# Performance work log

Measured on AMD Instinct MI355X. Metric: run time of the kernel, lower is better.

Reference implementation:

```python
import jax, jax.numpy as jnp
import numpy as np

T, N, E = 12, 100000, 3200000
F = H = 64
O, L = 32, 2


def setup_inputs() -> dict:
    key = jax.random.key(0)
    ks = jax.random.split(key, 13)
    sc = 0.08  # keep gate pre-activations in a sane range
    return {
        "x": jax.random.normal(ks[0], (T, N, F), jnp.float32),
        "hidden_states": jax.random.normal(ks[1], (L, N, H), jnp.float32),
        "cell_states": jax.random.normal(ks[2], (L, N, H), jnp.float32),
        "Wx_self": jax.random.normal(ks[3], (L, 4, F, H), jnp.float32) * sc,
        "Wx_neigh": jax.random.normal(ks[4], (L, 4, F, H), jnp.float32) * sc,
        "Wh_self": jax.random.normal(ks[5], (L, 4, H, H), jnp.float32) * sc,
        "Wh_neigh": jax.random.normal(ks[6], (L, 4, H, H), jnp.float32) * sc,
        "w_c": jax.random.normal(ks[7], (L, 3, H), jnp.float32) * sc,  # peephole i,f,o
        "bias": jax.random.normal(ks[8], (L, 4, H), jnp.float32) * sc,  # i,f,c,o
        "Wout": jax.random.normal(ks[9], (H, O), jnp.float32) * sc,
        "bout": jax.random.normal(ks[10], (O,), jnp.float32) * sc,
        "src": jax.random.randint(ks[11], (E,), 0, N, jnp.int32),
        "dst": jax.random.randint(ks[12], (E,), 0, N, jnp.int32),
    }


def reference(x, hidden_states, cell_states, Wx_self, Wx_neigh, Wh_self,
              Wh_neigh, w_c, bias, Wout, bout, src, dst):
    # mean aggregation over incoming edges (DGL copy_u + mean reduce)
    deg = jax.ops.segment_sum(jnp.ones((E,), x.dtype), dst, num_segments=N)
    deg_inv = jnp.where(deg > 0, 1.0 / deg, 0.0)[:, None]  # [N,1]

    def mean_agg(feat):  # [N,D] -> [N,D]
        return jax.ops.segment_sum(feat[src], dst, num_segments=N) * deg_inv

    def gates(feat, agg, Ws, Wn):  # Ws,Wn: [4,D,H] -> [4,N,H]
        return (jnp.einsum('nf,gfh->gnh', feat, Ws)
                + jnp.einsum('nf,gfh->gnh', agg, Wn))

    def step(carry, x_t):
        hs, cs = carry  # [L,N,H] each
        inp = x_t
        new_h, new_c = [], []
        for j in range(L):
            h, c = hs[j], cs[j]
            x_agg = mean_agg(inp)  # reuse_msg_passing: one agg shared by 4 gates
            h_agg = mean_agg(h)
            pre = gates(inp, x_agg, Wx_self[j], Wx_neigh[j]) \
                + gates(h, h_agg, Wh_self[j], Wh_neigh[j])  # [4,N,H]
            i = jax.nn.sigmoid(pre[0] + w_c[j, 0] * c + bias[j, 0])
            f = jax.nn.sigmoid(pre[1] + w_c[j, 1] * c + bias[j, 1])
            c_tilde = jnp.tanh(pre[2] + bias[j, 2])
            nc = f * c + i * c_tilde
            o = jax.nn.sigmoid(pre[3] + w_c[j, 2] * nc + bias[j, 3])
            nh = o * jnp.tanh(nc)
            new_h.append(nh)
            new_c.append(nc)
            inp = nh
        out_t = inp @ Wout + bout  # [N,O]
        return (jnp.stack(new_h), jnp.stack(new_c)), out_t

    (h_f, c_f), outs = jax.lax.scan(step, (hidden_states, cell_states), x)
    return outs, h_f, c_f  # outs: [T,N,O]
```

## Files before the change

kernel.cpp:

```cpp
#include <hip/hip_runtime.h>

#define T_STEPS 12
#define NN 100000
#define EE 3200000
#define HD 64
#define OD 32
#define NBK 391

typedef __attribute__((ext_vector_type(8))) short short8;
typedef __attribute__((ext_vector_type(4))) float f32x4;
typedef __attribute__((ext_vector_type(2))) float f32x2;
typedef unsigned short u16;
typedef unsigned char u8;

__device__ __forceinline__ u16 f2b(float x) {
  union { float f; unsigned u; } v; v.f = x;
  unsigned r = v.u + 0x7FFFu + ((v.u >> 16) & 1u);
  return (u16)(r >> 16);
}
__device__ __forceinline__ float b2f(u16 u) {
  union { unsigned u; float f; } v; v.u = ((unsigned)u) << 16;
  return v.f;
}
__device__ __forceinline__ float sigm(float x) {
  x = fminf(fmaxf(x, -30.f), 30.f);
  return 1.0f / (1.0f + __expf(-x));
}
__device__ __forceinline__ float tanh_f(float x) {
  x = fminf(fmaxf(x, -15.f), 15.f);
  float e = __expf(2.0f * x);
  return (e - 1.0f) / (e + 1.0f);
}

__device__ __forceinline__ uint2 pack8_fp8(const float* f) {
  unsigned lo = 0, hi = 0;
  lo = __builtin_amdgcn_cvt_pk_fp8_f32(f[0], f[1], lo, false);
  lo = __builtin_amdgcn_cvt_pk_fp8_f32(f[2], f[3], lo, true);
  hi = __builtin_amdgcn_cvt_pk_fp8_f32(f[4], f[5], hi, false);
  hi = __builtin_amdgcn_cvt_pk_fp8_f32(f[6], f[7], hi, true);
  return make_uint2(lo, hi);
}
__device__ __forceinline__ u8 f2q(float x) {
  return (u8)(__builtin_amdgcn_cvt_pk_fp8_f32(x, 0.f, 0u, false) & 0xFFu);
}
__device__ __forceinline__ void acc8_fp8(uint2 v, float* a) {
  f32x2 p0 = __builtin_amdgcn_cvt_pk_f32_fp8(v.x, false);
  f32x2 p1 = __builtin_amdgcn_cvt_pk_f32_fp8(v.x, true);
  f32x2 p2 = __builtin_amdgcn_cvt_pk_f32_fp8(v.y, false);
  f32x2 p3 = __builtin_amdgcn_cvt_pk_f32_fp8(v.y, true);
  a[0] += p0[0]; a[1] += p0[1]; a[2] += p1[0]; a[3] += p1[1];
  a[4] += p2[0]; a[5] += p2[1]; a[6] += p3[0]; a[7] += p3[1];
}

__global__ __launch_bounds__(256) void k_bhist(const int* __restrict__ dst,
                                               int* __restrict__ bcnt, int E) {
  __shared__ int h[NBK];
  for (int i = threadIdx.x; i < NBK; i += 256) h[i] = 0;
  __syncthreads();
  int base = blockIdx.x * 4096;
#pragma unroll
  for (int i = 0; i < 16; ++i) {
    int e = base + i * 256 + threadIdx.x;
    if (e < E) atomicAdd(&h[dst[e] >> 8], 1);
  }
  __syncthreads();
  for (int i = threadIdx.x; i < NBK; i += 256)
    if (h[i]) atomicAdd(&bcnt[i], h[i]);
}

__global__ __launch_bounds__(512) void k_bscan(const int* __restrict__ bcnt,
                                               int* __restrict__ bcur) {
  __shared__ int buf[512];
  int tid = threadIdx.x;
  int v = (tid < NBK) ? bcnt[tid] : 0;
  buf[tid] = v;
  __syncthreads();
  for (int off = 1; off < 512; off <<= 1) {
    int t = (tid >= off) ? buf[tid - off] : 0;
    __syncthreads();
    buf[tid] += t;
    __syncthreads();
  }
  if (tid < NBK) bcur[tid] = buf[tid] - v;
}

__global__ __launch_bounds__(256) void k_bscatter(const int* __restrict__ src,
                                                  const int* __restrict__ dst,
                                                  int* __restrict__ bcur,
                                                  uint2* __restrict__ binned, int E) {
  __shared__ int h[NBK];
  __shared__ int base[NBK];
  __shared__ int cur[NBK];
  for (int i = threadIdx.x; i < NBK; i += 256) { h[i] = 0; cur[i] = 0; }
  __syncthreads();
  int b0 = blockIdx.x * 4096;
  int d[16], s[16];
#pragma unroll
  for (int i = 0; i < 16; ++i) {
    int e = b0 + i * 256 + threadIdx.x;
    if (e < E) {
      d[i] = dst[e];
      s[i] = src[e];
      atomicAdd(&h[d[i] >> 8], 1);
    } else d[i] = -1;
  }
  __syncthreads();
  for (int i = threadIdx.x; i < NBK; i += 256)
    if (h[i]) base[i] = atomicAdd(&bcur[i], h[i]);
  __syncthreads();
#pragma unroll
  for (int i = 0; i < 16; ++i) {
    if (d[i] >= 0) {
      int bk = d[i] >> 8;
      int r = atomicAdd(&cur[bk], 1);
      binned[base[bk] + r] = make_uint2((unsigned)s[i], (unsigned)d[i]);
    }
  }
}

__global__ __launch_bounds__(256) void k_count2(const uint2* __restrict__ binned,
                                                int* __restrict__ deg, int E) {
  int e = blockIdx.x * 256 + threadIdx.x;
  if (e < E) atomicAdd(&deg[binned[e].y], 1);
}

__global__ __launch_bounds__(1024) void k_scanA(const int* __restrict__ deg,
                                                int* __restrict__ excl,
                                                int* __restrict__ btot, int n) {
  __shared__ int buf[1024];
  int tid = threadIdx.x;
  int i = blockIdx.x * 1024 + tid;
  int v = (i < n) ? deg[i] : 0;
  buf[tid] = v;
  __syncthreads();
  for (int off = 1; off < 1024; off <<= 1) {
    int t = (tid >= off) ? buf[tid - off] : 0;
    __syncthreads();
    buf[tid] += t;
    __syncthreads();
  }
  if (i < n) excl[i] = buf[tid] - v;
  if (tid == 1023) btot[blockIdx.x] = buf[1023];
}

__global__ __launch_bounds__(128) void k_scanB(const int* __restrict__ btot,
                                               int* __restrict__ boffs, int nb) {
  __shared__ int buf[128];
  int tid = threadIdx.x;
  int v = (tid < nb) ? btot[tid] : 0;
  buf[tid] = v;
  __syncthreads();
  for (int off = 1; off < 128; off <<= 1) {
    int t = (tid >= off) ? buf[tid - off] : 0;
    __syncthreads();
    buf[tid] += t;
    __syncthreads();
  }
  if (tid < nb) boffs[tid] = buf[tid] - v;
}

__global__ __launch_bounds__(1024) void k_scanC(const int* __restrict__ deg,
                                                const int* __restrict__ excl,
                                                const int* __restrict__ boffs,
                                                int* __restrict__ row_ptr,
                                                int* __restrict__ cursor,
                                                float* __restrict__ deg_inv, int n) {
  int i = blockIdx.x * 1024 + threadIdx.x;
  if (i < n) {
    int v = excl[i] + boffs[blockIdx.x];
    int d = deg[i];
    row_ptr[i] = v;
    cursor[i] = v;
    deg_inv[i] = d ? (1.0f / (float)d) : 0.0f;
    if (i == n - 1) row_ptr[n] = v + d;
  }
}

__global__ __launch_bounds__(256) void k_scatter2(const uint2* __restrict__ binned,
                                                  int* __restrict__ cursor,
                                                  int* __restrict__ csr, int E) {
  int e = blockIdx.x * 256 + threadIdx.x;
  if (e < E) {
    uint2 p = binned[e];
    int pos = atomicAdd(&cursor[p.y], 1);
    csr[pos] = (int)p.x;
  }
}

__global__ __launch_bounds__(256) void k_prep(const float* __restrict__ Wxs,
                                              const float* __restrict__ Wxn,
                                              const float* __restrict__ Whs,
                                              const float* __restrict__ Whn,
                                              u16* __restrict__ bprep) {
  int idx = blockIdx.x * 256 + threadIdx.x;
  int l = idx >> 16;
  int kb = (idx >> 13) & 7;
  int fi = (idx >> 9) & 15;
  int ln = (idx >> 3) & 63;
  int j = idx & 7;
  int fc = kb * 32 + ((ln >> 4) << 3) + j;
  int g = fi & 3;
  int kk = ((fi >> 2) << 4) + (ln & 15);
  int t = fc >> 6, f = fc & 63;
  const float* tabs[4] = {Wxs, Wxn, Whs, Whn};
  bprep[idx] = f2b(tabs[t][((size_t)(l * 4 + g) * 64 + f) * 64 + kk]);
}

__global__ __launch_bounds__(256) void k_prepw(const float* __restrict__ Wout,
                                               u16* __restrict__ wp) {
  int idx = blockIdx.x * 256 + threadIdx.x;
  int kb = idx >> 10;
  int fi = (idx >> 9) & 1;
  int ln = (idx >> 3) & 63;
  int j = idx & 7;
  int k = kb * 32 + ((ln >> 4) << 3) + j;
  int o = fi * 16 + (ln & 15);
  wp[idx] = f2b(Wout[k * 32 + o]);
}

__global__ __launch_bounds__(256) void k_convx(const float* __restrict__ x,
                                               u16* __restrict__ pa,
                                               u8* __restrict__ paq) {
  int idx = blockIdx.x * 256 + threadIdx.x;
  int n = idx >> 3, j = idx & 7;
  float4 v0 = *reinterpret_cast<const float4*>(x + (size_t)n * 64 + j * 8);
  float4 v1 = *reinterpret_cast<const float4*>(x + (size_t)n * 64 + j * 8 + 4);
  float f[8] = {v0.x, v0.y, v0.z, v0.w, v1.x, v1.y, v1.z, v1.w};
  short8 o;
#pragma unroll
  for (int i = 0; i < 8; ++i) o[i] = (short)f2b(f[i]);
  *reinterpret_cast<short8*>(pa + (size_t)n * 128 + j * 8) = o;
  *reinterpret_cast<uint2*>(paq + (size_t)n * 128 + j * 8) = pack8_fp8(f);
}

__global__ __launch_bounds__(256) void k_inith(const float* __restrict__ h0,
                                               u16* __restrict__ H0,
                                               u8* __restrict__ H0q,
                                               u16* __restrict__ PA,
                                               u8* __restrict__ PAq) {
  int idx = blockIdx.x * 256 + threadIdx.x;
  int n = idx >> 3, j = idx & 7;
#pragma unroll
  for (int L = 0; L < 2; ++L) {
    float4 v0 = *reinterpret_cast<const float4*>(h0 + (size_t)L * NN * 64 + (size_t)n * 64 + j * 8);
    float4 v1 = *reinterpret_cast<const float4*>(h0 + (size_t)L * NN * 64 + (size_t)n * 64 + j * 8 + 4);
    float f[8] = {v0.x, v0.y, v0.z, v0.w, v1.x, v1.y, v1.z, v1.w};
    short8 o;
#pragma unroll
    for (int i = 0; i < 8; ++i) o[i] = (short)f2b(f[i]);
    uint2 q = pack8_fp8(f);
    if (L == 0) {
      *reinterpret_cast<short8*>(H0 + (size_t)n * 64 + j * 8) = o;
      *reinterpret_cast<uint2*>(H0q + (size_t)n * 64 + j * 8) = q;
    } else {
      *reinterpret_cast<short8*>(PA + (size_t)n * 128 + 64 + j * 8) = o;
      *reinterpret_cast<uint2*>(PAq + (size_t)n * 128 + 64 + j * 8) = q;
    }
  }
}

__global__ __launch_bounds__(256) void k_agg_pair(const u8* __restrict__ Q,
                                                  const int* __restrict__ row_ptr,
                                                  const int* __restrict__ csr,
                                                  const float* __restrict__ deg_inv,
                                                  u16* __restrict__ outp) {
  int node = blockIdx.x * 4 + (threadIdx.x >> 6);
  int lane = threadIdx.x & 63;
  int g = lane >> 4, m = lane & 15;
  int start = row_ptr[node], end = row_ptr[node + 1];
  float a[8] = {0, 0, 0, 0, 0, 0, 0, 0};
  int e = start + g;
  for (; e + 12 < end; e += 16) {
    int s0 = csr[e], s1 = csr[e + 4], s2 = csr[e + 8], s3 = csr[e + 12];
    uint2 v0 = *reinterpret_cast<const uint2*>(Q + (size_t)s0 * 128 + m * 8);
    uint2 v1 = *reinterpret_cast<const uint2*>(Q + (size_t)s1 * 128 + m * 8);
    uint2 v2 = *reinterpret_cast<const uint2*>(Q + (size_t)s2 * 128 + m * 8);
    uint2 v3 = *reinterpret_cast<const uint2*>(Q + (size_t)s3 * 128 + m * 8);
    acc8_fp8(v0, a); acc8_fp8(v1, a); acc8_fp8(v2, a); acc8_fp8(v3, a);
  }
  if (e + 4 < end) {
    int s0 = csr[e], s1 = csr[e + 4];
    uint2 v0 = *reinterpret_cast<const uint2*>(Q + (size_t)s0 * 128 + m * 8);
    uint2 v1 = *reinterpret_cast<const uint2*>(Q + (size_t)s1 * 128 + m * 8);
    acc8_fp8(v0, a); acc8_fp8(v1, a);
    e += 8;
  }
  if (e < end) {
    int s0 = csr[e];
    uint2 v0 = *reinterpret_cast<const uint2*>(Q + (size_t)s0 * 128 + m * 8);
    acc8_fp8(v0, a);
  }
#pragma unroll
  for (int off = 16; off < 64; off <<= 1) {
#pragma unroll
    for (int i = 0; i < 8; ++i) a[i] += __shfl_xor(a[i], off);
  }
  if (g == 0) {
    float sc = deg_inv[node];
    short8 o;
#pragma unroll
    for (int i = 0; i < 8; ++i) o[i] = (short)f2b(a[i] * sc);
    *reinterpret_cast<short8*>(outp + (size_t)node * 128 + m * 8) = o;
  }
}

__global__ __launch_bounds__(256) void k_agg_single(const u8* __restrict__ Q,
                                                    const int* __restrict__ row_ptr,
                                                    const int* __restrict__ csr,
                                                    const float* __restrict__ deg_inv,
                                                    u16* __restrict__ outp) {
  int node = blockIdx.x * 4 + (threadIdx.x >> 6);
  int lane = threadIdx.x & 63;
  int g = lane >> 3, m = lane & 7;
  int start = row_ptr[node], end = row_ptr[node + 1];
  float a[8] = {0, 0, 0, 0, 0, 0, 0, 0};
  int e = start + g;
  for (; e + 24 < end; e += 32) {
    int s0 = csr[e], s1 = csr[e + 8], s2 = csr[e + 16], s3 = csr[e + 24];
    uint2 v0 = *reinterpret_cast<const uint2*>(Q + (size_t)s0 * 64 + m * 8);
    uint2 v1 = *reinterpret_cast<const uint2*>(Q + (size_t)s1 * 64 + m * 8);
    uint2 v2 = *reinterpret_cast<const uint2*>(Q + (size_t)s2 * 64 + m * 8);
    uint2 v3 = *reinterpret_cast<const uint2*>(Q + (size_t)s3 * 64 + m * 8);
    acc8_fp8(v0, a); acc8_fp8(v1, a); acc8_fp8(v2, a); acc8_fp8(v3, a);
  }
  if (e + 8 < end) {
    int s0 = csr[e], s1 = csr[e + 8];
    uint2 v0 = *reinterpret_cast<const uint2*>(Q + (size_t)s0 * 64 + m * 8);
    uint2 v1 = *reinterpret_cast<const uint2*>(Q + (size_t)s1 * 64 + m * 8);
    acc8_fp8(v0, a); acc8_fp8(v1, a);
    e += 16;
  }
  if (e < end) {
    int s0 = csr[e];
    uint2 v0 = *reinterpret_cast<const uint2*>(Q + (size_t)s0 * 64 + m * 8);
    acc8_fp8(v0, a);
  }
#pragma unroll
  for (int off = 8; off < 64; off <<= 1) {
#pragma unroll
    for (int i = 0; i < 8; ++i) a[i] += __shfl_xor(a[i], off);
  }
  if (g == 0) {
    float sc = deg_inv[node];
    short8 o;
#pragma unroll
    for (int i = 0; i < 8; ++i) o[i] = (short)f2b(a[i] * sc);
    *reinterpret_cast<short8*>(outp + (size_t)node * 64 + m * 8) = o;
  }
}

__global__ __launch_bounds__(256, 2) void k_gates(
    const u16* __restrict__ tab0, const u16* __restrict__ tab1,
    u16* __restrict__ tab2, const u16* __restrict__ tab3,
    int ld0, int ld1, int ld2, int ld3,
    u8* __restrict__ qtab2, int qld,
    float* __restrict__ cst, float* __restrict__ hf32,
    const u16* __restrict__ bprepl,
    const float* __restrict__ wcl, const float* __restrict__ biasl,
    const u16* __restrict__ wproj, const float* __restrict__ boutp,
    float* __restrict__ outp,
    int n_nodes, int writef32, int doproj) {
  __shared__ u16 Hsm[64 * 64];
  const int tid = threadIdx.x;
  const int lane = tid & 63;
  const int w = tid >> 6;
  const int nb = blockIdx.x * 64;
  const int cl = lane & 15;
  const int kg = lane >> 4;

  short8 breg[8][4];
#pragma unroll
  for (int kb = 0; kb < 8; ++kb)
#pragma unroll
    for (int fl = 0; fl < 4; ++fl)
      breg[kb][fl] = *reinterpret_cast<const short8*>(
          bprepl + (kb << 13) + (((w << 2) + fl) << 9) + (lane << 3));

  const u16* tabs[4] = {tab0, tab1, tab2, tab3};
  const int lds[4] = {ld0, ld1, ld2, ld3};
  int gnc[4];
#pragma unroll
  for (int rg = 0; rg < 4; ++rg) {
    int g = nb + rg * 16 + cl;
    gnc[rg] = (g < n_nodes) ? g : (n_nodes - 1);
  }

  f32x4 acc[4][4];
  f32x4 z4 = {0.f, 0.f, 0.f, 0.f};
#pragma unroll
  for (int a = 0; a < 4; ++a)
#pragma unroll
    for (int b = 0; b < 4; ++b) acc[a][b] = z4;

  const int koff = kg << 3;
#pragma unroll
  for (int kb = 0; kb < 8; ++kb) {
    const u16* tp = tabs[kb >> 1];
    const int ld = lds[kb >> 1];
    const int idx = ((kb & 1) << 5) + koff;
#pragma unroll
    for (int rg = 0; rg < 4; ++rg) {
      short8 a = *reinterpret_cast<const short8*>(tp + (size_t)gnc[rg] * ld + idx);
      acc[rg][0] = __builtin_amdgcn_mfma_f32_16x16x32_bf16(a, breg[kb][0], acc[rg][0], 0, 0, 0);
      acc[rg][1] = __builtin_amdgcn_mfma_f32_16x16x32_bf16(a, breg[kb][1], acc[rg][1], 0, 0, 0);
      acc[rg][2] = __builtin_amdgcn_mfma_f32_16x16x32_bf16(a, breg[kb][2], acc[rg][2], 0, 0, 0);
      acc[rg][3] = __builtin_amdgcn_mfma_f32_16x16x32_bf16(a, breg[kb][3], acc[rg][3], 0, 0, 0);
    }
  }

  const int k = (w << 4) + cl;
  const float wci = wcl[k], wcf = wcl[64 + k], wco = wcl[128 + k];
  const float bi = biasl[k], bfg = biasl[64 + k], bc = biasl[128 + k], bo = biasl[192 + k];
#pragma unroll
  for (int rg = 0; rg < 4; ++rg) {
#pragma unroll
    for (int r = 0; r < 4; ++r) {
      int n = nb + rg * 16 + kg * 4 + r;
      if (n < n_nodes) {
        size_t off = (size_t)n * 64 + k;
        float c_old = cst[off];
        float ig = sigm(acc[rg][0][r] + wci * c_old + bi);
        float fg = sigm(acc[rg][1][r] + wcf * c_old + bfg);
        float ct = tanh_f(acc[rg][2][r] + bc);
        float nc = fg * c_old + ig * ct;
        float og = sigm(acc[rg][3][r] + wco * nc + bo);
        float nh = og * tanh_f(nc);
        cst[off] = nc;
        u16 hb = f2b(nh);
        tab2[(size_t)n * ld2 + k] = hb;
        qtab2[(size_t)n * qld + k] = f2q(nh);
        if (doproj) Hsm[(rg * 16 + kg * 4 + r) * 64 + k] = hb;
        if (writef32) hf32[off] = nh;
      }
    }
  }

  if (doproj) {
    __syncthreads();
    short8 bw[2][2];
#pragma unroll
    for (int kb = 0; kb < 2; ++kb)
#pragma unroll
      for (int fi = 0; fi < 2; ++fi)
        bw[kb][fi] = *reinterpret_cast<const short8*>(wproj + (((kb * 2 + fi) * 64 + lane) << 3));
    short8 a0 = *reinterpret_cast<const short8*>(&Hsm[(w * 16 + cl) * 64 + kg * 8]);
    short8 a1 = *reinterpret_cast<const short8*>(&Hsm[(w * 16 + cl) * 64 + 32 + kg * 8]);
    f32x4 p0 = z4, p1 = z4;
    p0 = __builtin_amdgcn_mfma_f32_16x16x32_bf16(a0, bw[0][0], p0, 0, 0, 0);
    p0 = __builtin_amdgcn_mfma_f32_16x16x32_bf16(a1, bw[1][0], p0, 0, 0, 0);
    p1 = __builtin_amdgcn_mfma_f32_16x16x32_bf16(a0, bw[0][1], p1, 0, 0, 0);
    p1 = __builtin_amdgcn_mfma_f32_16x16x32_bf16(a1, bw[1][1], p1, 0, 0, 0);
    const float bo0 = boutp[cl], bo1 = boutp[16 + cl];
#pragma unroll
    for (int r = 0; r < 4; ++r) {
      int n = nb + w * 16 + kg * 4 + r;
      if (n < n_nodes) {
        outp[(size_t)n * OD + cl] = p0[r] + bo0;
        outp[(size_t)n * OD + 16 + cl] = p1[r] + bo1;
      }
    }
  }
}

extern "C" void kernel_launch(void* const* d_in, const int* in_sizes, int n_in,
                              void* d_out, int out_size, void* d_ws, size_t ws_size,
                              hipStream_t stream) {
  const float* x = (const float*)d_in[0];
  const float* h0 = (const float*)d_in[1];
  const float* c0 = (const float*)d_in[2];
  const float* Wxs = (const float*)d_in[3];
  const float* Wxn = (const float*)d_in[4];
  const float* Whs = (const float*)d_in[5];
  const float* Whn = (const float*)d_in[6];
  const float* wc = (const float*)d_in[7];
  const float* bias = (const float*)d_in[8];
  const float* Wout = (const float*)d_in[9];
  const float* bout = (const float*)d_in[10];
  const int* src = (const int*)d_in[11];
  const int* dst = (const int*)d_in[12];

  float* out = (float*)d_out;
  float* outs = out;
  float* hstate = out + (size_t)T_STEPS * NN * OD;
  float* cstate = hstate + (size_t)2 * NN * HD;

  char* p = (char*)d_ws;
  auto alloc = [&](size_t bytes) {
    char* r = p;
    p += (bytes + 255) & ~(size_t)255;
    return r;
  };
  int* csr = (int*)alloc((size_t)EE * 4);
  uint2* binned = (uint2*)alloc((size_t)EE * 8);
  int* row_ptr = (int*)alloc((size_t)(NN + 1) * 4);
  int* cursor = (int*)alloc((size_t)NN * 4);
  int* deg = (int*)alloc((size_t)NN * 4);
  int* excl = (int*)alloc((size_t)NN * 4);
  int* btot = (int*)alloc(128 * 4);
  int* boffs = (int*)alloc(128 * 4);
  int* bcnt = (int*)alloc(NBK * 4);
  int* bcur = (int*)alloc(NBK * 4);
  float* deg_inv = (float*)alloc((size_t)NN * 4);
  u16* PA = (u16*)alloc((size_t)NN * 128 * 2);
  u8* PAq = (u8*)alloc((size_t)NN * 128);
  u16* H0 = (u16*)alloc((size_t)NN * 64 * 2);
  u8* H0q = (u8*)alloc((size_t)NN * 64);
  u16* AGGP = (u16*)alloc((size_t)NN * 128 * 2);
  u16* AGGH = (u16*)alloc((size_t)NN * 64 * 2);
  u16* bprep = (u16*)alloc((size_t)2 * 65536 * 2);
  u16* wprep = (u16*)alloc((size_t)2048 * 2);

  const int nscan = (NN + 1023) / 1024;
  const int nchunk = (EE + 4095) / 4096;

  hipMemsetAsync(deg, 0, (size_t)NN * 4, stream);
  hipMemsetAsync(bcnt, 0, (size_t)NBK * 4, stream);
  k_bhist<<<nchunk, 256, 0, stream>>>(dst, bcnt, EE);
  k_bscan<<<1, 512, 0, stream>>>(bcnt, bcur);
  k_bscatter<<<nchunk, 256, 0, stream>>>(src, dst, bcur, binned, EE);
  k_count2<<<(EE + 255) / 256, 256, 0, stream>>>(binned, deg, EE);
  k_scanA<<<nscan, 1024, 0, stream>>>(deg, excl, btot, NN);
  k_scanB<<<1, 128, 0, stream>>>(btot, boffs, nscan);
  k_scanC<<<nscan, 1024, 0, stream>>>(deg, excl, boffs, row_ptr, cursor, deg_inv, NN);
  k_scatter2<<<(EE + 255) / 256, 256, 0, stream>>>(binned, cursor, csr, EE);
  k_prep<<<512, 256, 0, stream>>>(Wxs, Wxn, Whs, Whn, bprep);
  k_prepw<<<8, 256, 0, stream>>>(Wout, wprep);
  k_inith<<<NN * 8 / 256, 256, 0, stream>>>(h0, H0, H0q, PA, PAq);
  hipMemcpyAsync(cstate, c0, (size_t)2 * NN * HD * 4, hipMemcpyDeviceToDevice, stream);
  k_agg_single<<<NN / 4, 256, 0, stream>>>(H0q, row_ptr, csr, deg_inv, AGGH);

  for (int t = 0; t < T_STEPS; ++t) {
    int wf = (t == T_STEPS - 1) ? 1 : 0;
    k_convx<<<NN * 8 / 256, 256, 0, stream>>>(x + (size_t)t * NN * HD, PA, PAq);
    k_agg_pair<<<NN / 4, 256, 0, stream>>>(PAq, row_ptr, csr, deg_inv, AGGP);
    k_gates<<<(NN + 63) / 64, 256, 0, stream>>>(
        PA, AGGP, H0, AGGH, 128, 128, 64, 64,
        H0q, 64,
        cstate, hstate, bprep, wc, bias,
        wprep, bout, nullptr, NN, wf, 0);
    k_agg_single<<<NN / 4, 256, 0, stream>>>(H0q, row_ptr, csr, deg_inv, AGGH);
    k_gates<<<(NN + 63) / 64, 256, 0, stream>>>(
        H0, AGGH, PA + 64, AGGP + 64, 64, 64, 128, 128,
        PAq + 64, 128,
        cstate + (size_t)NN * HD, hstate + (size_t)NN * HD,
        bprep + 65536, wc + 192, bias + 256,
        wprep, bout, outs + (size_t)t * NN * OD, NN, wf, 1);
  }
}
```

Baseline: 3.140 ms.

## Hoist input aggregation for all timesteps and merge hidden-state aggregations per step

The input features do not depend on the recurrence, so all timesteps are converted to fp8 once and their neighbour means are computed in a single gather pass over a node-major [N, T*64] layout. The per-step loop then runs only one paired aggregation, covering the freshly updated layer-0 hidden state and the previous layer-1 hidden state. This removes the per-step x conversion and one of the two gather kernels per step. The gates kernel is split into layer-specialised versions that read fp32 x directly. In exchange, the aggregated x is stored as fp8 rather than bf16, which adds quantisation error, and the edge-binning scratch buffer is now aliased with the x buffer.

```diff
diff --git a/kernel.cpp b/kernel.cpp
--- a/kernel.cpp
+++ b/kernel.cpp
@@ -17,10 +17,6 @@
   union { float f; unsigned u; } v; v.f = x;
   unsigned r = v.u + 0x7FFFu + ((v.u >> 16) & 1u);
   return (u16)(r >> 16);
-}
-__device__ __forceinline__ float b2f(u16 u) {
-  union { unsigned u; float f; } v; v.u = ((unsigned)u) << 16;
-  return v.f;
 }
 __device__ __forceinline__ float sigm(float x) {
   x = fminf(fmaxf(x, -30.f), 30.f);
@@ -50,6 +46,37 @@
   f32x2 p3 = __builtin_amdgcn_cvt_pk_f32_fp8(v.y, true);
   a[0] += p0[0]; a[1] += p0[1]; a[2] += p1[0]; a[3] += p1[1];
   a[4] += p2[0]; a[5] += p2[1]; a[6] += p3[0]; a[7] += p3[1];
+}
+__device__ __forceinline__ void dec16_acc(uint4 q, float* a) {
+  f32x2 t;
+  t = __builtin_amdgcn_cvt_pk_f32_fp8(q.x, false); a[0] += t[0]; a[1] += t[1];
+  t = __builtin_amdgcn_cvt_pk_f32_fp8(q.x, true);  a[2] += t[0]; a[3] += t[1];
+  t = __builtin_amdgcn_cvt_pk_f32_fp8(q.y, false); a[4] += t[0]; a[5] += t[1];
+  t = __builtin_amdgcn_cvt_pk_f32_fp8(q.y, true);  a[6] += t[0]; a[7] += t[1];
+  t = __builtin_amdgcn_cvt_pk_f32_fp8(q.z, false); a[8] += t[0]; a[9] += t[1];
+  t = __builtin_amdgcn_cvt_pk_f32_fp8(q.z, true);  a[10] += t[0]; a[11] += t[1];
+  t = __builtin_amdgcn_cvt_pk_f32_fp8(q.w, false); a[12] += t[0]; a[13] += t[1];
+  t = __builtin_amdgcn_cvt_pk_f32_fp8(q.w, true);  a[14] += t[0]; a[15] += t[1];
+}
+__device__ __forceinline__ short8 s8_from_fp8(uint2 q) {
+  f32x2 p0 = __builtin_amdgcn_cvt_pk_f32_fp8(q.x, false);
+  f32x2 p1 = __builtin_amdgcn_cvt_pk_f32_fp8(q.x, true);
+  f32x2 p2 = __builtin_amdgcn_cvt_pk_f32_fp8(q.y, false);
+  f32x2 p3 = __builtin_amdgcn_cvt_pk_f32_fp8(q.y, true);
+  short8 o;
+  o[0] = (short)f2b(p0[0]); o[1] = (short)f2b(p0[1]);
+  o[2] = (short)f2b(p1[0]); o[3] = (short)f2b(p1[1]);
+  o[4] = (short)f2b(p2[0]); o[5] = (short)f2b(p2[1]);
+  o[6] = (short)f2b(p3[0]); o[7] = (short)f2b(p3[1]);
+  return o;
+}
+__device__ __forceinline__ short8 s8_from_f32(float4 a, float4 b) {
+  short8 o;
+  o[0] = (short)f2b(a.x); o[1] = (short)f2b(a.y);
+  o[2] = (short)f2b(a.z); o[3] = (short)f2b(a.w);
+  o[4] = (short)f2b(b.x); o[5] = (short)f2b(b.y);
+  o[6] = (short)f2b(b.z); o[7] = (short)f2b(b.w);
+  return o;
 }
 
 __global__ __launch_bounds__(256) void k_bhist(const int* __restrict__ dst,
@@ -218,43 +245,104 @@
   wp[idx] = f2b(Wout[k * 32 + o]);
 }
 
-__global__ __launch_bounds__(256) void k_convx(const float* __restrict__ x,
-                                               u16* __restrict__ pa,
-                                               u8* __restrict__ paq) {
+__global__ __launch_bounds__(256) void k_convxall(const float* __restrict__ x,
+                                                  u8* __restrict__ XQ) {
+  int tid = blockIdx.x * 256 + threadIdx.x;
+  int j = tid & 7;
+  int tn = tid >> 3;
+  int n = tn % NN;
+  int t = tn / NN;
+  const float* rp = x + (size_t)tn * 64 + j * 8;
+  float4 v0 = *reinterpret_cast<const float4*>(rp);
+  float4 v1 = *reinterpret_cast<const float4*>(rp + 4);
+  float f[8] = {v0.x, v0.y, v0.z, v0.w, v1.x, v1.y, v1.z, v1.w};
+  *reinterpret_cast<uint2*>(XQ + (size_t)n * 768 + t * 64 + j * 8) = pack8_fp8(f);
+}
+
+__global__ __launch_bounds__(256) void k_inith(const float* __restrict__ h0,
+                                               u16* __restrict__ H0bf,
+                                               u16* __restrict__ L1bf,
+                                               u8* __restrict__ HQ) {
   int idx = blockIdx.x * 256 + threadIdx.x;
   int n = idx >> 3, j = idx & 7;
-  float4 v0 = *reinterpret_cast<const float4*>(x + (size_t)n * 64 + j * 8);
-  float4 v1 = *reinterpret_cast<const float4*>(x + (size_t)n * 64 + j * 8 + 4);
-  float f[8] = {v0.x, v0.y, v0.z, v0.w, v1.x, v1.y, v1.z, v1.w};
-  short8 o;
-#pragma unroll
-  for (int i = 0; i < 8; ++i) o[i] = (short)f2b(f[i]);
-  *reinterpret_cast<short8*>(pa + (size_t)n * 128 + j * 8) = o;
-  *reinterpret_cast<uint2*>(paq + (size_t)n * 128 + j * 8) = pack8_fp8(f);
-}
-
-__global__ __launch_bounds__(256) void k_inith(const float* __restrict__ h0,
-                                               u16* __restrict__ H0,
-                                               u8* __restrict__ H0q,
-                                               u16* __restrict__ PA,
-                                               u8* __restrict__ PAq) {
-  int idx = blockIdx.x * 256 + threadIdx.x;
-  int n = idx >> 3, j = idx & 7;
 #pragma unroll
   for (int L = 0; L < 2; ++L) {
-    float4 v0 = *reinterpret_cast<const float4*>(h0 + (size_t)L * NN * 64 + (size_t)n * 64 + j * 8);
-    float4 v1 = *reinterpret_cast<const float4*>(h0 + (size_t)L * NN * 64 + (size_t)n * 64 + j * 8 + 4);
+    const float* rp = h0 + (size_t)L * NN * 64 + (size_t)n * 64 + j * 8;
+    float4 v0 = *reinterpret_cast<const float4*>(rp);
+    float4 v1 = *reinterpret_cast<const float4*>(rp + 4);
     float f[8] = {v0.x, v0.y, v0.z, v0.w, v1.x, v1.y, v1.z, v1.w};
     short8 o;
 #pragma unroll
     for (int i = 0; i < 8; ++i) o[i] = (short)f2b(f[i]);
-    uint2 q = pack8_fp8(f);
-    if (L == 0) {
-      *reinterpret_cast<short8*>(H0 + (size_t)n * 64 + j * 8) = o;
-      *reinterpret_cast<uint2*>(H0q + (size_t)n * 64 + j * 8) = q;
-    } else {
-      *reinterpret_cast<short8*>(PA + (size_t)n * 128 + 64 + j * 8) = o;
-      *reinterpret_cast<uint2*>(PAq + (size_t)n * 128 + 64 + j * 8) = q;
+    if (L == 0)
+      *reinterpret_cast<short8*>(H0bf + (size_t)n * 64 + j * 8) = o;
+    else
+      *reinterpret_cast<short8*>(L1bf + (size_t)n * 64 + j * 8) = o;
+    *reinterpret_cast<uint2*>(HQ + (size_t)n * 128 + L * 64 + j * 8) = pack8_fp8(f);
+  }
+}
+
+__global__ __launch_bounds__(256) void k_aggx(const u8* __restrict__ XQ,
+                                              const int* __restrict__ row_ptr,
+                                              const int* __restrict__ csr,
+                                              const float* __restrict__ deg_inv,
+                                              u8* __restrict__ AGGXq) {
+  int node = blockIdx.x * 4 + (threadIdx.x >> 6);
+  int lane = threadIdx.x & 63;
+  int g = lane >> 4, m = lane & 15;
+  int start = row_ptr[node], end = row_ptr[node + 1];
+  float acc[3][16];
+#pragma unroll
+  for (int p = 0; p < 3; ++p)
+#pragma unroll
+    for (int i = 0; i < 16; ++i) acc[p][i] = 0.f;
+  int e = start + g;
+  for (; e + 4 < end; e += 8) {
+    int s0 = csr[e], s1 = csr[e + 4];
+    const u8* r0 = XQ + (size_t)s0 * 768 + m * 16;
+    const u8* r1 = XQ + (size_t)s1 * 768 + m * 16;
+#pragma unroll
+    for (int p = 0; p < 3; ++p) {
+      uint4 q0 = *reinterpret_cast<const uint4*>(r0 + p * 256);
+      uint4 q1 = *reinterpret_cast<const uint4*>(r1 + p * 256);
+      dec16_acc(q0, acc[p]);
+      dec16_acc(q1, acc[p]);
+    }
+  }
+  if (e < end) {
+    int s0 = csr[e];
+    const u8* r0 = XQ + (size_t)s0 * 768 + m * 16;
+#pragma unroll
+    for (int p = 0; p < 3; ++p) {
+      uint4 q0 = *reinterpret_cast<const uint4*>(r0 + p * 256);
+      dec16_acc(q0, acc[p]);
+    }
+  }
+#pragma unroll
+  for (int off = 16; off < 64; off <<= 1)
+#pragma unroll
+    for (int p = 0; p < 3; ++p)
+#pragma unroll
+      for (int i = 0; i < 16; ++i) acc[p][i] += __shfl_xor(acc[p][i], off);
+  if (g == 0) {
+    float sc = deg_inv[node];
+#pragma unroll
+    for (int p = 0; p < 3; ++p) {
+      float f[16];
+#pragma unroll
+      for (int i = 0; i < 16; ++i) f[i] = acc[p][i] * sc;
+      uint4 o;
+      unsigned w;
+      w = 0; w = __builtin_amdgcn_cvt_pk_fp8_f32(f[0], f[1], w, false);
+      w = __builtin_amdgcn_cvt_pk_fp8_f32(f[2], f[3], w, true); o.x = w;
+      w = 0; w = __builtin_amdgcn_cvt_pk_fp8_f32(f[4], f[5], w, false);
+      w = __builtin_amdgcn_cvt_pk_fp8_f32(f[6], f[7], w, true); o.y = w;
+      w = 0; w = __builtin_amdgcn_cvt_pk_fp8_f32(f[8], f[9], w, false);
+      w = __builtin_amdgcn_cvt_pk_fp8_f32(f[10], f[11], w, true); o.z = w;
+      w = 0; w = __builtin_amdgcn_cvt_pk_fp8_f32(f[12], f[13], w, false);
+      w = __builtin_amdgcn_cvt_pk_fp8_f32(f[14], f[15], w, true); o.w = w;
+      int t = p * 4 + (m >> 2);
+      *reinterpret_cast<uint4*>(AGGXq + ((size_t)t * NN + node) * 64 + (m & 3) * 16) = o;
     }
   }
 }
@@ -304,62 +392,101 @@
   }
 }
 
-__global__ __launch_bounds__(256) void k_agg_single(const u8* __restrict__ Q,
-                                                    const int* __restrict__ row_ptr,
-                                                    const int* __restrict__ csr,
-                                                    const float* __restrict__ deg_inv,
-                                                    u16* __restrict__ outp) {
-  int node = blockIdx.x * 4 + (threadIdx.x >> 6);
-  int lane = threadIdx.x & 63;
-  int g = lane >> 3, m = lane & 7;
-  int start = row_ptr[node], end = row_ptr[node + 1];
-  float a[8] = {0, 0, 0, 0, 0, 0, 0, 0};
-  int e = start + g;
-  for (; e + 24 < end; e += 32) {
-    int s0 = csr[e], s1 = csr[e + 8], s2 = csr[e + 16], s3 = csr[e + 24];
-    uint2 v0 = *reinterpret_cast<const uint2*>(Q + (size_t)s0 * 64 + m * 8);
-    uint2 v1 = *reinterpret_cast<const uint2*>(Q + (size_t)s1 * 64 + m * 8);
-    uint2 v2 = *reinterpret_cast<const uint2*>(Q + (size_t)s2 * 64 + m * 8);
-    uint2 v3 = *reinterpret_cast<const uint2*>(Q + (size_t)s3 * 64 + m * 8);
-    acc8_fp8(v0, a); acc8_fp8(v1, a); acc8_fp8(v2, a); acc8_fp8(v3, a);
-  }
-  if (e + 8 < end) {
-    int s0 = csr[e], s1 = csr[e + 8];
-    uint2 v0 = *reinterpret_cast<const uint2*>(Q + (size_t)s0 * 64 + m * 8);
-    uint2 v1 = *reinterpret_cast<const uint2*>(Q + (size_t)s1 * 64 + m * 8);
-    acc8_fp8(v0, a); acc8_fp8(v1, a);
-    e += 16;
-  }
-  if (e < end) {
-    int s0 = csr[e];
-    uint2 v0 = *reinterpret_cast<const uint2*>(Q + (size_t)s0 * 64 + m * 8);
-    acc8_fp8(v0, a);
-  }
-#pragma unroll
-  for (int off = 8; off < 64; off <<= 1) {
-#pragma unroll
-    for (int i = 0; i < 8; ++i) a[i] += __shfl_xor(a[i], off);
-  }
-  if (g == 0) {
-    float sc = deg_inv[node];
-    short8 o;
-#pragma unroll
-    for (int i = 0; i < 8; ++i) o[i] = (short)f2b(a[i] * sc);
-    *reinterpret_cast<short8*>(outp + (size_t)node * 64 + m * 8) = o;
-  }
-}
-
-__global__ __launch_bounds__(256, 2) void k_gates(
-    const u16* __restrict__ tab0, const u16* __restrict__ tab1,
-    u16* __restrict__ tab2, const u16* __restrict__ tab3,
-    int ld0, int ld1, int ld2, int ld3,
-    u8* __restrict__ qtab2, int qld,
+__global__ __launch_bounds__(256, 2) void k_gates0(
+    const float* __restrict__ xin, const u8* __restrict__ aggxq,
+    u16* __restrict__ h0bf, const u16* __restrict__ agghl,
+    u8* __restrict__ hq, float* __restrict__ cst, float* __restrict__ hf32,
+    const u16* __restrict__ bprepl,
+    const float* __restrict__ wcl, const float* __restrict__ biasl,
+    int n_nodes, int writef32) {
+  const int tid = threadIdx.x;
+  const int lane = tid & 63;
+  const int w = tid >> 6;
+  const int nb = blockIdx.x * 64;
+  const int cl = lane & 15;
+  const int kg = lane >> 4;
+
+  short8 breg[8][4];
+#pragma unroll
+  for (int kb = 0; kb < 8; ++kb)
+#pragma unroll
+    for (int fl = 0; fl < 4; ++fl)
+      breg[kb][fl] = *reinterpret_cast<const short8*>(
+          bprepl + (kb << 13) + (((w << 2) + fl) << 9) + (lane << 3));
+
+  int gnc[4];
+#pragma unroll
+  for (int rg = 0; rg < 4; ++rg) {
+    int g = nb + rg * 16 + cl;
+    gnc[rg] = (g < n_nodes) ? g : (n_nodes - 1);
+  }
+
+  f32x4 acc[4][4];
+  f32x4 z4 = {0.f, 0.f, 0.f, 0.f};
+#pragma unroll
+  for (int a = 0; a < 4; ++a)
+#pragma unroll
+    for (int b = 0; b < 4; ++b) acc[a][b] = z4;
+
+  const int koff = kg << 3;
+#pragma unroll
+  for (int kb = 0; kb < 8; ++kb) {
+    const int idx = ((kb & 1) << 5) + koff;
+#pragma unroll
+    for (int rg = 0; rg < 4; ++rg) {
+      short8 a;
+      if (kb < 2) {
+        const float* rp = xin + (size_t)gnc[rg] * 64 + idx;
+        a = s8_from_f32(*reinterpret_cast<const float4*>(rp),
+                        *reinterpret_cast<const float4*>(rp + 4));
+      } else if (kb < 4) {
+        a = s8_from_fp8(*reinterpret_cast<const uint2*>(aggxq + (size_t)gnc[rg] * 64 + idx));
+      } else if (kb < 6) {
+        a = *reinterpret_cast<const short8*>(h0bf + (size_t)gnc[rg] * 64 + idx);
+      } else {
+        a = *reinterpret_cast<const short8*>(agghl + (size_t)gnc[rg] * 128 + idx);
+      }
+      acc[rg][0] = __builtin_amdgcn_mfma_f32_16x16x32_bf16(a, breg[kb][0], acc[rg][0], 0, 0, 0);
+      acc[rg][1] = __builtin_amdgcn_mfma_f32_16x16x32_bf16(a, breg[kb][1], acc[rg][1], 0, 0, 0);
+      acc[rg][2] = __builtin_amdgcn_mfma_f32_16x16x32_bf16(a, breg[kb][2], acc[rg][2], 0, 0, 0);
+      acc[rg][3] = __builtin_amdgcn_mfma_f32_16x16x32_bf16(a, breg[kb][3], acc[rg][3], 0, 0, 0);
+    }
+  }
+
+  const int k = (w << 4) + cl;
+  const float wci = wcl[k], wcf = wcl[64 + k], wco = wcl[128 + k];
+  const float bi = biasl[k], bfg = biasl[64 + k], bc = biasl[128 + k], bo = biasl[192 + k];
+#pragma unroll
+  for (int rg = 0; rg < 4; ++rg) {
+#pragma unroll
+    for (int r = 0; r < 4; ++r) {
+      int n = nb + rg * 16 + kg * 4 + r;
+      if (n < n_nodes) {
+        size_t off = (size_t)n * 64 + k;
+        float c_old = cst[off];
+        float ig = sigm(acc[rg][0][r] + wci * c_old + bi);
+        float fg = sigm(acc[rg][1][r] + wcf * c_old + bfg);
+        float ct = tanh_f(acc[rg][2][r] + bc);
+        float nc = fg * c_old + ig * ct;
+        float og = sigm(acc[rg][3][r] + wco * nc + bo);
+        float nh = og * tanh_f(nc);
+        cst[off] = nc;
+        h0bf[off] = f2b(nh);
+        hq[(size_t)n * 128 + k] = f2q(nh);
+        if (writef32) hf32[off] = nh;
+      }
+    }
+  }
+}
+
+__global__ __launch_bounds__(256, 2) void k_gates1(
+    const u16* __restrict__ h0bf, const u16* __restrict__ agghl,
+    u16* __restrict__ l1bf, u8* __restrict__ hq,
     float* __restrict__ cst, float* __restrict__ hf32,
     const u16* __restrict__ bprepl,
     const float* __restrict__ wcl, const float* __restrict__ biasl,
     const u16* __restrict__ wproj, const float* __restrict__ boutp,
-    float* __restrict__ outp,
-    int n_nodes, int writef32, int doproj) {
+    float* __restrict__ outp, int n_nodes, int writef32) {
   __shared__ u16 Hsm[64 * 64];
   const int tid = threadIdx.x;
   const int lane = tid & 63;
@@ -376,8 +503,6 @@
       breg[kb][fl] = *reinterpret_cast<const short8*>(
           bprepl + (kb << 13) + (((w << 2) + fl) << 9) + (lane << 3));
 
-  const u16* tabs[4] = {tab0, tab1, tab2, tab3};
-  const int lds[4] = {ld0, ld1, ld2, ld3};
   int gnc[4];
 #pragma unroll
   for (int rg = 0; rg < 4; ++rg) {
@@ -395,12 +520,19 @@
   const int koff = kg << 3;
 #pragma unroll
   for (int kb = 0; kb < 8; ++kb) {
-    const u16* tp = tabs[kb >> 1];
-    const int ld = lds[kb >> 1];
     const int idx = ((kb & 1) << 5) + koff;
 #pragma unroll
     for (int rg = 0; rg < 4; ++rg) {
-      short8 a = *reinterpret_cast<const short8*>(tp + (size_t)gnc[rg] * ld + idx);
+      short8 a;
+      if (kb < 2) {
+        a = *reinterpret_cast<const short8*>(h0bf + (size_t)gnc[rg] * 64 + idx);
+      } else if (kb < 4) {
+        a = *reinterpret_cast<const short8*>(agghl + (size_t)gnc[rg] * 128 + idx);
+      } else if (kb < 6) {
+        a = *reinterpret_cast<const short8*>(l1bf + (size_t)gnc[rg] * 64 + idx);
+      } else {
+        a = *reinterpret_cast<const short8*>(agghl + (size_t)gnc[rg] * 128 + 64 + idx);
+      }
       acc[rg][0] = __builtin_amdgcn_mfma_f32_16x16x32_bf16(a, breg[kb][0], acc[rg][0], 0, 0, 0);
       acc[rg][1] = __builtin_amdgcn_mfma_f32_16x16x32_bf16(a, breg[kb][1], acc[rg][1], 0, 0, 0);
       acc[rg][2] = __builtin_amdgcn_mfma_f32_16x16x32_bf16(a, breg[kb][2], acc[rg][2], 0, 0, 0);
@@ -427,37 +559,35 @@
         float nh = og * tanh_f(nc);
         cst[off] = nc;
         u16 hb = f2b(nh);
-        tab2[(size_t)n * ld2 + k] = hb;
-        qtab2[(size_t)n * qld + k] = f2q(nh);
-        if (doproj) Hsm[(rg * 16 + kg * 4 + r) * 64 + k] = hb;
+        l1bf[off] = hb;
+        hq[(size_t)n * 128 + 64 + k] = f2q(nh);
+        Hsm[(rg * 16 + kg * 4 + r) * 64 + k] = hb;
         if (writef32) hf32[off] = nh;
       }
     }
   }
 
-  if (doproj) {
-    __syncthreads();
-    short8 bw[2][2];
-#pragma unroll
-    for (int kb = 0; kb < 2; ++kb)
-#pragma unroll
-      for (int fi = 0; fi < 2; ++fi)
-        bw[kb][fi] = *reinterpret_cast<const short8*>(wproj + (((kb * 2 + fi) * 64 + lane) << 3));
-    short8 a0 = *reinterpret_cast<const short8*>(&Hsm[(w * 16 + cl) * 64 + kg * 8]);
-    short8 a1 = *reinterpret_cast<const short8*>(&Hsm[(w * 16 + cl) * 64 + 32 + kg * 8]);
-    f32x4 p0 = z4, p1 = z4;
-    p0 = __builtin_amdgcn_mfma_f32_16x16x32_bf16(a0, bw[0][0], p0, 0, 0, 0);
-    p0 = __builtin_amdgcn_mfma_f32_16x16x32_bf16(a1, bw[1][0], p0, 0, 0, 0);
-    p1 = __builtin_amdgcn_mfma_f32_16x16x32_bf16(a0, bw[0][1], p1, 0, 0, 0);
-    p1 = __builtin_amdgcn_mfma_f32_16x16x32_bf16(a1, bw[1][1], p1, 0, 0, 0);
-    const float bo0 = boutp[cl], bo1 = boutp[16 + cl];
-#pragma unroll
-    for (int r = 0; r < 4; ++r) {
-      int n = nb + w * 16 + kg * 4 + r;
-      if (n < n_nodes) {
-        outp[(size_t)n * OD + cl] = p0[r] + bo0;
-        outp[(size_t)n * OD + 16 + cl] = p1[r] + bo1;
-      }
+  __syncthreads();
+  short8 bw[2][2];
+#pragma unroll
+  for (int kb = 0; kb < 2; ++kb)
+#pragma unroll
+    for (int fi = 0; fi < 2; ++fi)
+      bw[kb][fi] = *reinterpret_cast<const short8*>(wproj + (((kb * 2 + fi) * 64 + lane) << 3));
+  short8 a0 = *reinterpret_cast<const short8*>(&Hsm[(w * 16 + cl) * 64 + kg * 8]);
+  short8 a1 = *reinterpret_cast<const short8*>(&Hsm[(w * 16 + cl) * 64 + 32 + kg * 8]);
+  f32x4 p0 = z4, p1 = z4;
+  p0 = __builtin_amdgcn_mfma_f32_16x16x32_bf16(a0, bw[0][0], p0, 0, 0, 0);
+  p0 = __builtin_amdgcn_mfma_f32_16x16x32_bf16(a1, bw[1][0], p0, 0, 0, 0);
+  p1 = __builtin_amdgcn_mfma_f32_16x16x32_bf16(a0, bw[0][1], p1, 0, 0, 0);
+  p1 = __builtin_amdgcn_mfma_f32_16x16x32_bf16(a1, bw[1][1], p1, 0, 0, 0);
+  const float bo0 = boutp[cl], bo1 = boutp[16 + cl];
+#pragma unroll
+  for (int r = 0; r < 4; ++r) {
+    int n = nb + w * 16 + kg * 4 + r;
+    if (n < n_nodes) {
+      outp[(size_t)n * OD + cl] = p0[r] + bo0;
+      outp[(size_t)n * OD + 16 + cl] = p1[r] + bo1;
     }
   }
 }
@@ -491,7 +621,9 @@
     return r;
   };
   int* csr = (int*)alloc((size_t)EE * 4);
-  uint2* binned = (uint2*)alloc((size_t)EE * 8);
+  u8* XQ = (u8*)alloc((size_t)NN * 768);
+  uint2* binned = (uint2*)XQ;
+  u8* AGGXq = (u8*)alloc((size_t)T_STEPS * NN * 64);
   int* row_ptr = (int*)alloc((size_t)(NN + 1) * 4);
   int* cursor = (int*)alloc((size_t)NN * 4);
   int* deg = (int*)alloc((size_t)NN * 4);
@@ -501,12 +633,10 @@
   int* bcnt = (int*)alloc(NBK * 4);
   int* bcur = (int*)alloc(NBK * 4);
   float* deg_inv = (float*)alloc((size_t)NN * 4);
-  u16* PA = (u16*)alloc((size_t)NN * 128 * 2);
-  u8* PAq = (u8*)alloc((size_t)NN * 128);
-  u16* H0 = (u16*)alloc((size_t)NN * 64 * 2);
-  u8* H0q = (u8*)alloc((size_t)NN * 64);
-  u16* AGGP = (u16*)alloc((size_t)NN * 128 * 2);
-  u16* AGGH = (u16*)alloc((size_t)NN * 64 * 2);
+  u16* H0bf = (u16*)alloc((size_t)NN * 64 * 2);
+  u16* L1bf = (u16*)alloc((size_t)NN * 64 * 2);
+  u8* HQ = (u8*)alloc((size_t)NN * 128);
+  u16* AGGHL = (u16*)alloc((size_t)NN * 128 * 2);
   u16* bprep = (u16*)alloc((size_t)2 * 65536 * 2);
   u16* wprep = (u16*)alloc((size_t)2048 * 2);
 
@@ -525,25 +655,22 @@
   k_scatter2<<<(EE + 255) / 256, 256, 0, stream>>>(binned, cursor, csr, EE);
   k_prep<<<512, 256, 0, stream>>>(Wxs, Wxn, Whs, Whn, bprep);
   k_prepw<<<8, 256, 0, stream>>>(Wout, wprep);
-  k_inith<<<NN * 8 / 256, 256, 0, stream>>>(h0, H0, H0q, PA, PAq);
+  k_convxall<<<(T_STEPS * NN * 8 + 255) / 256, 256, 0, stream>>>(x, XQ);
+  k_inith<<<NN * 8 / 256, 256, 0, stream>>>(h0, H0bf, L1bf, HQ);
   hipMemcpyAsync(cstate, c0, (size_t)2 * NN * HD * 4, hipMemcpyDeviceToDevice, stream);
-  k_agg_single<<<NN / 4, 256, 0, stream>>>(H0q, row_ptr, csr, deg_inv, AGGH);
+  k_aggx<<<(NN + 3) / 4, 256, 0, stream>>>(XQ, row_ptr, csr, deg_inv, AGGXq);
+  k_agg_pair<<<(NN + 3) / 4, 256, 0, stream>>>(HQ, row_ptr, csr, deg_inv, AGGHL);
 
   for (int t = 0; t < T_STEPS; ++t) {
     int wf = (t == T_STEPS - 1) ? 1 : 0;
-    k_convx<<<NN * 8 / 256, 256, 0, stream>>>(x + (size_t)t * NN * HD, PA, PAq);
-    k_agg_pair<<<NN / 4, 256, 0, stream>>>(PAq, row_ptr, csr, deg_inv, AGGP);
-    k_gates<<<(NN + 63) / 64, 256, 0, stream>>>(
-        PA, AGGP, H0, AGGH, 128, 128, 64, 64,
-        H0q, 64,
-        cstate, hstate, bprep, wc, bias,
-        wprep, bout, nullptr, NN, wf, 0);
-    k_agg_single<<<NN / 4, 256, 0, stream>>>(H0q, row_ptr, csr, deg_inv, AGGH);
-    k_gates<<<(NN + 63) / 64, 256, 0, stream>>>(
-        H0, AGGH, PA + 64, AGGP + 64, 64, 64, 128, 128,
-        PAq + 64, 128,
+    k_gates0<<<(NN + 63) / 64, 256, 0, stream>>>(
+        x + (size_t)t * NN * HD, AGGXq + (size_t)t * NN * 64,
+        H0bf, AGGHL, HQ, cstate, hstate, bprep, wc, bias, NN, wf);
+    k_agg_pair<<<(NN + 3) / 4, 256, 0, stream>>>(HQ, row_ptr, csr, deg_inv, AGGHL);
+    k_gates1<<<(NN + 63) / 64, 256, 0, stream>>>(
+        H0bf, AGGHL, L1bf, HQ,
         cstate + (size_t)NN * HD, hstate + (size_t)NN * HD,
         bprep + 65536, wc + 192, bias + 256,
-        wprep, bout, outs + (size_t)t * NN * OD, NN, wf, 1);
-  }
-}
+        wprep, bout, outs + (size_t)t * NN * OD, NN, wf);
+  }
+}
```

Measured after the change: 2.998 ms. 1.05x faster.
